# Performance work log

Measured on AMD Instinct MI355X. Metric: run time of the kernel, lower is better.

## Reference

```python
import jax, jax.numpy as jnp
import numpy as np

N_NODES = 10000
N_EDGES = 640000
F_NODE = 128   # n_node_features
F_EDGE = 128   # hiddens (edge_attr width)


def setup_inputs() -> dict:
    key = jax.random.key(0)
    k1, k2, k3, k4 = jax.random.split(key, 4)
    x = jax.random.normal(k1, (N_NODES, F_NODE), dtype=jnp.float32)
    edge_index = jax.random.randint(k2, (2, N_EDGES), 0, N_NODES, dtype=jnp.int64)
    edge_attr = jax.random.normal(k3, (N_EDGES, F_EDGE), dtype=jnp.float32)
    u = jax.random.normal(k4, (1, 16), dtype=jnp.float32)
    batch = jnp.zeros((N_NODES,), dtype=jnp.int64)
    return {"x": x, "edge_index": edge_index, "edge_attr": edge_attr, "u": u, "batch": batch}


def reference(x, edge_index, edge_attr, u, batch):
    # row: destination (scatter target), col: source (gather index)
    row, col = edge_index[0], edge_index[1]
    n = x.shape[0]
    # [E, F_NODE + F_EDGE]: gather source node feats, concat edge feats
    msg = jnp.concatenate([x[col], edge_attr], axis=1)
    # scatter_mean over destination nodes (count clamped to 1, matching torch_scatter)
    summed = jax.ops.segment_sum(msg, row, num_segments=n)
    counts = jax.ops.segment_sum(jnp.ones((row.shape[0],), x.dtype), row, num_segments=n)
    mean = summed / jnp.maximum(counts, 1.0)[:, None]
    # [N, 2*F_NODE + F_EDGE]
    return jnp.concatenate([x, mean], axis=1)
```

## Files before the change

kernel.cpp:

```cpp
#include <hip/hip_runtime.h>

#define F      128
#define OUT_W  384
#define NBLK   128
#define HT     512

typedef __attribute__((ext_vector_type(4))) float f4;

__global__ __launch_bounds__(HT) void hist_kernel(const int* __restrict__ row,
                                                  int* __restrict__ hist,
                                                  int E, int N, int chunk) {
    extern __shared__ int h[];
    const int t = threadIdx.x;
    for (int i = t; i < N; i += HT) h[i] = 0;
    __syncthreads();
    const int lo = blockIdx.x * chunk;
    const int hi = min(lo + chunk, E);
    for (int i = lo + t; i < hi; i += HT) atomicAdd(&h[row[i]], 1);
    __syncthreads();
    int* dst = hist + (size_t)blockIdx.x * N;
    for (int i = t; i < N; i += HT) dst[i] = h[i];
}

__global__ void totals_kernel(const int* __restrict__ hist, int* __restrict__ tot, int N) {
    const int n = blockIdx.x * blockDim.x + threadIdx.x;
    if (n >= N) return;
    int s = 0;
    for (int b = 0; b < NBLK; ++b) s += hist[(size_t)b * N + n];
    tot[n] = s;
}

__global__ __launch_bounds__(1024) void scan_kernel(const int* __restrict__ tot,
                                                    int* __restrict__ offsets, int N) {
    const int t = threadIdx.x;
    const int chunk = (N + 1023) / 1024;
    const int lo = min(t * chunk, N);
    const int hi = min(lo + chunk, N);
    int local = 0;
    for (int i = lo; i < hi; ++i) local += tot[i];
    const int lane = t & 63, wv = t >> 6;
    int incl = local;
    for (int d = 1; d < 64; d <<= 1) {
        int v = __shfl_up(incl, d);
        if (lane >= d) incl += v;
    }
    __shared__ int wsum[16];
    if (lane == 63) wsum[wv] = incl;
    __syncthreads();
    int wpre = 0;
    for (int w = 0; w < wv; ++w) wpre += wsum[w];
    int run = wpre + incl - local;
    for (int i = lo; i < hi; ++i) { offsets[i] = run; run += tot[i]; }
    if (t == 1023) offsets[N] = wpre + incl;
}

__global__ void blockstart_kernel(int* hist, const int* __restrict__ offsets, int N) {
    const int n = blockIdx.x * blockDim.x + threadIdx.x;
    if (n >= N) return;
    int run = offsets[n];
    for (int b = 0; b < NBLK; ++b) {
        const size_t k = (size_t)b * N + n;
        const int v = hist[k];
        hist[k] = run;
        run += v;
    }
}

__global__ __launch_bounds__(HT) void scatter_kernel(const int* __restrict__ row,
                                                     const int* __restrict__ col,
                                                     const int* __restrict__ hist,
                                                     int* __restrict__ eid,
                                                     int* __restrict__ cid,
                                                     int E, int N, int chunk) {
    extern __shared__ int cur[];
    const int t = threadIdx.x;
    const int* src = hist + (size_t)blockIdx.x * N;
    for (int i = t; i < N; i += HT) cur[i] = src[i];
    __syncthreads();
    const int lo = blockIdx.x * chunk;
    const int hi = min(lo + chunk, E);
    for (int i = lo + t; i < hi; i += HT) {
        const int r = row[i];
        const int p = atomicAdd(&cur[r], 1);
        eid[p] = i;
        cid[p] = col[i];
    }
}

template <bool NT>
__device__ __forceinline__ void accum_half(const float* __restrict__ mat,
                                           const int* __restrict__ list,
                                           int start, int end, int lane, f4& acc) {
    const int which = lane >> 5;
    const int sub   = lane & 31;
    for (int base = start; base < end; base += 64) {
        const int m = min(64, end - base);
        int idx = base + lane;
        if (idx >= end) idx = end - 1;
        const int myid = list[idx];
        const int full = m & ~1;
        for (int i = 0; i < full; i += 2) {
            const int id = __shfl(myid, i + which);
            const f4* p = (const f4*)(mat + (size_t)id * F + sub * 4);
            const f4 v = NT ? __builtin_nontemporal_load(p) : *p;
            acc += v;
        }
        if (m & 1) {
            const int id = __shfl(myid, full);
            if (which == 0) {
                const f4* p = (const f4*)(mat + (size_t)id * F + sub * 4);
                const f4 v = NT ? __builtin_nontemporal_load(p) : *p;
                acc += v;
            }
        }
    }
}

__global__ __launch_bounds__(256) void aggregate_kernel(
    const float* __restrict__ x, const float* __restrict__ edge_attr,
    const int* __restrict__ offsets, const int* __restrict__ eid,
    const int* __restrict__ cid, float* __restrict__ out, int N) {

    const int wave = threadIdx.x >> 6;
    const int lane = threadIdx.x & 63;
    const int wid  = blockIdx.x * 4 + wave;
    const int node = wid >> 1;
    const int half = wid & 1;
    if (node >= N) return;

    const int start = offsets[node];
    const int end   = offsets[node + 1];

    f4 acc = {0.f, 0.f, 0.f, 0.f};
    if (half == 0) accum_half<false>(x,         cid, start, end, lane, acc);
    else           accum_half<true >(edge_attr, eid, start, end, lane, acc);

    acc.x += __shfl_xor(acc.x, 32);
    acc.y += __shfl_xor(acc.y, 32);
    acc.z += __shfl_xor(acc.z, 32);
    acc.w += __shfl_xor(acc.w, 32);

    const float inv = 1.0f / fmaxf((float)(end - start), 1.0f);
    const int which = lane >> 5, sub = lane & 31;
    float* orow = out + (size_t)node * OUT_W;

    if (half == 0) {
        if (which == 0) {
            f4 mean = {acc.x * inv, acc.y * inv, acc.z * inv, acc.w * inv};
            *(f4*)(orow + F + sub * 4) = mean;
        } else {
            *(f4*)(orow + sub * 4) =
                *(const f4*)(x + (size_t)node * F + sub * 4);
        }
    } else if (which == 0) {
        f4 mean = {acc.x * inv, acc.y * inv, acc.z * inv, acc.w * inv};
        *(f4*)(orow + 2 * F + sub * 4) = mean;
    }
}

extern "C" void kernel_launch(void* const* d_in, const int* in_sizes, int n_in,
                              void* d_out, int out_size, void* d_ws, size_t ws_size,
                              hipStream_t stream) {
    const float* x          = (const float*)d_in[0];
    const int*   edge_index = (const int*)d_in[1];
    const float* edge_attr  = (const float*)d_in[2];

    const int N = in_sizes[0] / F;
    const int E = in_sizes[1] / 2;
    const int* row = edge_index;
    const int* col = edge_index + E;

    int* hist    = (int*)d_ws;
    int* tot     = hist + (size_t)NBLK * N;
    int* offsets = tot + N;
    int* eid     = offsets + N + 1;
    int* cid     = eid + E;

    float* out = (float*)d_out;

    const int chunk  = (E + NBLK - 1) / NBLK;
    const size_t smem = (size_t)N * sizeof(int);

    hist_kernel      <<<NBLK, HT, smem, stream>>>(row, hist, E, N, chunk);
    totals_kernel    <<<(N + 255) / 256, 256, 0, stream>>>(hist, tot, N);
    scan_kernel      <<<1, 1024, 0, stream>>>(tot, offsets, N);
    blockstart_kernel<<<(N + 255) / 256, 256, 0, stream>>>(hist, offsets, N);
    scatter_kernel   <<<NBLK, HT, smem, stream>>>(row, col, hist, eid, cid, E, N, chunk);
    aggregate_kernel <<<(2 * N + 3) / 4, 256, 0, stream>>>(x, edge_attr, offsets,
                                                           eid, cid, out, N);
}
```

Before: 512.3 us.

## Drop sorted col array, unroll gather loop, and halve histogram blocks

The scatter kernel no longer writes a permuted copy of the source indices. The aggregate kernel instead looks up col through the sorted edge ids, which adds an indirect gather in exchange for one less scattered write stream. The gather loop is unrolled four pairs deep so more row loads are in flight at once. The histogram/scatter block count drops from 128 to 64, which shrinks the per-block histogram work but gives fewer blocks for the edge passes.

```diff
diff --git a/kernel.cpp b/kernel.cpp
--- a/kernel.cpp
+++ b/kernel.cpp
@@ -2,7 +2,7 @@
 
 #define F      128
 #define OUT_W  384
-#define NBLK   128
+#define NBLK   64
 #define HT     512
 
 typedef __attribute__((ext_vector_type(4))) float f4;
@@ -67,10 +67,8 @@
 }
 
 __global__ __launch_bounds__(HT) void scatter_kernel(const int* __restrict__ row,
-                                                     const int* __restrict__ col,
                                                      const int* __restrict__ hist,
                                                      int* __restrict__ eid,
-                                                     int* __restrict__ cid,
                                                      int E, int N, int chunk) {
     extern __shared__ int cur[];
     const int t = threadIdx.x;
@@ -80,16 +78,21 @@
     const int lo = blockIdx.x * chunk;
     const int hi = min(lo + chunk, E);
     for (int i = lo + t; i < hi; i += HT) {
-        const int r = row[i];
-        const int p = atomicAdd(&cur[r], 1);
+        const int p = atomicAdd(&cur[row[i]], 1);
         eid[p] = i;
-        cid[p] = col[i];
-    }
+    }
+}
+
+template <bool NT>
+__device__ __forceinline__ f4 row_ld(const float* __restrict__ mat, int id, int sub) {
+    const f4* p = (const f4*)(mat + (size_t)id * F + sub * 4);
+    return NT ? __builtin_nontemporal_load(p) : *p;
 }
 
 template <bool NT>
 __device__ __forceinline__ void accum_half(const float* __restrict__ mat,
-                                           const int* __restrict__ list,
+                                           const int* __restrict__ eid,
+                                           const int* __restrict__ colmap,
                                            int start, int end, int lane, f4& acc) {
     const int which = lane >> 5;
     const int sub   = lane & 31;
@@ -97,29 +100,36 @@
         const int m = min(64, end - base);
         int idx = base + lane;
         if (idx >= end) idx = end - 1;
-        const int myid = list[idx];
+        int myid = eid[idx];
+        if (colmap) myid = colmap[myid];
+        int i = 0;
+        for (; i + 8 <= m; i += 8) {
+            const int id0 = __shfl(myid, i + 0 + which);
+            const int id1 = __shfl(myid, i + 2 + which);
+            const int id2 = __shfl(myid, i + 4 + which);
+            const int id3 = __shfl(myid, i + 6 + which);
+            const f4 v0 = row_ld<NT>(mat, id0, sub);
+            const f4 v1 = row_ld<NT>(mat, id1, sub);
+            const f4 v2 = row_ld<NT>(mat, id2, sub);
+            const f4 v3 = row_ld<NT>(mat, id3, sub);
+            acc += v0; acc += v1; acc += v2; acc += v3;
+        }
         const int full = m & ~1;
-        for (int i = 0; i < full; i += 2) {
+        for (; i < full; i += 2) {
             const int id = __shfl(myid, i + which);
-            const f4* p = (const f4*)(mat + (size_t)id * F + sub * 4);
-            const f4 v = NT ? __builtin_nontemporal_load(p) : *p;
-            acc += v;
+            acc += row_ld<NT>(mat, id, sub);
         }
         if (m & 1) {
             const int id = __shfl(myid, full);
-            if (which == 0) {
-                const f4* p = (const f4*)(mat + (size_t)id * F + sub * 4);
-                const f4 v = NT ? __builtin_nontemporal_load(p) : *p;
-                acc += v;
-            }
+            if (which == 0) acc += row_ld<NT>(mat, id, sub);
         }
     }
 }
 
 __global__ __launch_bounds__(256) void aggregate_kernel(
     const float* __restrict__ x, const float* __restrict__ edge_attr,
-    const int* __restrict__ offsets, const int* __restrict__ eid,
-    const int* __restrict__ cid, float* __restrict__ out, int N) {
+    const int* __restrict__ col, const int* __restrict__ offsets,
+    const int* __restrict__ eid, float* __restrict__ out, int N) {
 
     const int wave = threadIdx.x >> 6;
     const int lane = threadIdx.x & 63;
@@ -132,8 +142,8 @@
     const int end   = offsets[node + 1];
 
     f4 acc = {0.f, 0.f, 0.f, 0.f};
-    if (half == 0) accum_half<false>(x,         cid, start, end, lane, acc);
-    else           accum_half<true >(edge_attr, eid, start, end, lane, acc);
+    if (half == 0) accum_half<false>(x,         eid, col,     start, end, lane, acc);
+    else           accum_half<true >(edge_attr, eid, nullptr, start, end, lane, acc);
 
     acc.x += __shfl_xor(acc.x, 32);
     acc.y += __shfl_xor(acc.y, 32);
@@ -174,7 +184,6 @@
     int* tot     = hist + (size_t)NBLK * N;
     int* offsets = tot + N;
     int* eid     = offsets + N + 1;
-    int* cid     = eid + E;
 
     float* out = (float*)d_out;
 
@@ -185,7 +194,7 @@
     totals_kernel    <<<(N + 255) / 256, 256, 0, stream>>>(hist, tot, N);
     scan_kernel      <<<1, 1024, 0, stream>>>(tot, offsets, N);
     blockstart_kernel<<<(N + 255) / 256, 256, 0, stream>>>(hist, offsets, N);
-    scatter_kernel   <<<NBLK, HT, smem, stream>>>(row, col, hist, eid, cid, E, N, chunk);
-    aggregate_kernel <<<(2 * N + 3) / 4, 256, 0, stream>>>(x, edge_attr, offsets,
-                                                           eid, cid, out, N);
-}
+    scatter_kernel   <<<NBLK, HT, smem, stream>>>(row, hist, eid, E, N, chunk);
+    aggregate_kernel <<<(2 * N + 3) / 4, 256, 0, stream>>>(x, edge_attr, col,
+                                                           offsets, eid, out, N);
+}
```

Result: faster. 486.8 us (-5.0%).
